# Performance work log

Hardware: AMD Instinct MI355X
Metric: run time of the kernel (lower is better)

The kernel has to match this reference:

```python
import jax, jax.numpy as jnp
import numpy as np

ALPHA = 0.2        # LeakyReLU negative slope
MASK_VAL = -9e15   # matches torch -9000000000000000.0


def setup_inputs() -> dict:
    key = jax.random.key(0)
    k_h, k_adj, k_w, k_a = jax.random.split(key, 4)
    B, N, Nodes, IF, OF = 8, 8, 512, 256, 256
    h = jax.random.normal(k_h, (B, N, Nodes, IF), dtype=jnp.float32)
    adj = jax.random.randint(k_adj, (Nodes, Nodes), 0, 2, dtype=jnp.int32)
    # xavier_uniform with gain=1.414
    gain = 1.414
    lim_w = gain * np.sqrt(6.0 / (IF + OF))
    W = jax.random.uniform(k_w, (IF, OF), dtype=jnp.float32, minval=-lim_w, maxval=lim_w)
    lim_a = gain * np.sqrt(6.0 / (2 * OF + 1))
    a = jax.random.uniform(k_a, (2 * OF, 1), dtype=jnp.float32, minval=-lim_a, maxval=lim_a)
    return {"h": h, "adj": adj, "W": W, "a": a}


def reference(h, adj, W, a):
    # Wh: [B, N, Nodes, OF]
    Wh = jnp.matmul(h, W)
    OF = W.shape[1]
    a1, a2 = a[:OF, 0], a[OF:, 0]
    # e[..., i, j] = leakyrelu(a1 . Wh_i + a2 . Wh_j)  (decomposed additive attention)
    src = jnp.einsum('bnif,f->bni', Wh, a1)  # [B, N, Nodes]
    dst = jnp.einsum('bnjf,f->bnj', Wh, a2)  # [B, N, Nodes]
    e = jax.nn.leaky_relu(src[..., :, None] + dst[..., None, :], negative_slope=ALPHA)
    attention = jnp.where(adj > 0, e, jnp.full_like(e, MASK_VAL))
    attention = jax.nn.softmax(attention, axis=-1)
    # dropout is identity in eval mode (training=False)
    h_prime = jnp.matmul(attention, Wh)  # [B, N, Nodes, OF]
    return jax.nn.elu(h_prime)  # concat=True
```

## Files before the change

### kernel.cpp

```cpp
#include <hip/hip_runtime.h>
#include <hip/hip_bf16.h>


#define ALPHA 0.2f
#define MASK_VAL -9000000000000000.0f
#define NODES 512
#define FDIM 256
#define BN 64

typedef float  f32x4 __attribute__((ext_vector_type(4)));
typedef int    i32x4 __attribute__((ext_vector_type(4)));
typedef short  s16x8 __attribute__((ext_vector_type(8)));
typedef short  s16x4 __attribute__((ext_vector_type(4)));
typedef __bf16 bf16x8 __attribute__((ext_vector_type(8)));

__device__ __forceinline__ unsigned short f2bfu(float x) {
    __hip_bfloat16 b = __float2bfloat16(x);
    unsigned short u; __builtin_memcpy(&u, &b, 2); return u;
}
__device__ __forceinline__ float bfu2f(unsigned short u) {
    unsigned int w = ((unsigned int)u) << 16; return __uint_as_float(w);
}
__device__ __forceinline__ f32x4 mfma16(s16x8 a, s16x8 b, f32x4 c) {
    return __builtin_amdgcn_mfma_f32_16x16x32_bf16(
        __builtin_bit_cast(bf16x8, a), __builtin_bit_cast(bf16x8, b), c, 0, 0, 0);
}

__device__ __forceinline__ void split8v(f32x4 v0, f32x4 v1, s16x8& hi, s16x8& lo)
{
    float x[8] = {v0[0], v0[1], v0[2], v0[3], v1[0], v1[1], v1[2], v1[3]};
    unsigned hw[4], lw[4];
    #pragma unroll
    for (int d = 0; d < 4; ++d) {
        const unsigned u0 = __float_as_uint(x[2*d]);
        const unsigned u1 = __float_as_uint(x[2*d + 1]);
        hw[d] = __builtin_amdgcn_perm(u1, u0, 0x07060302);
        const float l0 = x[2*d]     - __uint_as_float(u0 & 0xFFFF0000u);
        const float l1 = x[2*d + 1] - __uint_as_float(u1 & 0xFFFF0000u);
        lw[d] = __builtin_amdgcn_perm(__float_as_uint(l1), __float_as_uint(l0),
                                      0x07060302);
    }
    hi = __builtin_bit_cast(s16x8, *(unsigned(*)[4])hw);
    lo = __builtin_bit_cast(s16x8, *(unsigned(*)[4])lw);
}

__device__ __forceinline__ void gll16(const void* g, void* l) {
    __builtin_amdgcn_global_load_lds(
        (const __attribute__((address_space(1))) unsigned int*)g,
        (__attribute__((address_space(3))) unsigned int*)l,
        16, 0, 0);
}

__global__ __launch_bounds__(256) void detect_kernel(const unsigned short* __restrict__ hraw,
                                                     int* __restrict__ flag)
{
    const int tid = threadIdx.x;
    float m = 0.0f;
    for (int i = tid; i < 16384; i += 256) {
        unsigned int w = ((unsigned int)hraw[i]) << 16;
        float v = __uint_as_float(w);
        v = fabsf(v);
        if (!(v == v)) v = 1e30f;
        m = fmaxf(m, v);
    }
    #pragma unroll
    for (int off = 32; off >= 1; off >>= 1)
        m = fmaxf(m, __shfl_down(m, off));
    __shared__ float red[4];
    if ((tid & 63) == 0) red[tid >> 6] = m;
    __syncthreads();
    if (tid == 0) {
        float mm = fmaxf(fmaxf(red[0], red[1]), fmaxf(red[2], red[3]));
        *flag = (mm > 1e4f) ? 1 : 0;
    }
}

__global__ __launch_bounds__(256) void prep_w_kernel(
    const void* __restrict__ Wv, const int* __restrict__ flagp,
    short* __restrict__ WtHi, short* __restrict__ WtLo)
{
    const int flag = *flagp;
    __shared__ float tile[16][17];
    const int tx = threadIdx.x & 15, ty = threadIdx.x >> 4;
    const int kk = blockIdx.y * 16 + ty;
    const int f  = blockIdx.x * 16 + tx;
    float v;
    if (flag) v = ((const float*)Wv)[kk * FDIM + f];
    else      v = bfu2f(((const unsigned short*)Wv)[kk * FDIM + f]);
    tile[ty][tx] = v;
    __syncthreads();
    const float x = tile[tx][ty];
    const int fo = blockIdx.x * 16 + ty;
    const int ko = blockIdx.y * 16 + tx;
    unsigned short h = f2bfu(x);
    WtHi[fo * FDIM + ko] = (short)h;
    WtLo[fo * FDIM + ko] = (short)f2bfu(x - bfu2f(h));
}

__global__ __launch_bounds__(512, 4) void wh_gemm(
    const void* __restrict__ hv,
    const short* __restrict__ WtHi, const short* __restrict__ WtLo,
    const void* __restrict__ av, const int* __restrict__ flagp,
    short* __restrict__ WhTHi, short* __restrict__ WhTLo,
    float* __restrict__ srcv, float* __restrict__ dstv)
{
    __shared__ __align__(16) char smem[69632];

    const int flag = *flagp;
    const int blk = blockIdx.x;
    const int bn  = blk >> 3;
    const int i0  = (blk & 7) * 64;
    const size_t r0g = (size_t)blk * 64;
    const int tid = threadIdx.x;
    const int w = tid >> 6, l = tid & 63;
    const int fb = l & 15, g = l >> 4;

    if (flag) {
        const int srow = tid >> 3, q = tid & 7;
        const float* gA = (const float*)hv + (r0g + srow) * FDIM;
        #pragma unroll
        for (int i = 0; i < 4; ++i) {
            const int seg = q + 8 * i;
            f32x4 v0 = *(const f32x4*)(gA + seg * 8);
            f32x4 v1 = *(const f32x4*)(gA + seg * 8 + 4);
            s16x8 hi, lo; split8v(v0, v1, hi, lo);
            const int slot = seg ^ (srow & 7);
            *(s16x8*)(smem + srow * 512 + slot * 16) = hi;
            *(s16x8*)(smem + 32768 + srow * 512 + slot * 16) = lo;
        }
    } else {
        const short* hs = (const short*)hv;
        const unsigned wub = (unsigned)(tid & ~63);
        #pragma unroll
        for (int i = 0; i < 4; ++i) {
            const int idx = i * 512 + tid;
            const int row = idx >> 5, slot = idx & 31;
            const int srcseg = slot ^ (row & 7);
            gll16(hs + (r0g + row) * FDIM + srcseg * 8,
                  smem + (i * 512 + (int)wub) * 16);
        }
    }
    __syncthreads();

    f32x4 acc[4][2];
    #pragma unroll
    for (int rt = 0; rt < 4; ++rt)
        #pragma unroll
        for (int ct = 0; ct < 2; ++ct) acc[rt][ct] = f32x4{0.f,0.f,0.f,0.f};

    const int f0 = w * 32 + fb;
    const int f1 = f0 + 16;
    const short* gH0 = WtHi + f0 * FDIM + g * 8;
    const short* gH1 = WtHi + f1 * FDIM + g * 8;
    const short* gL0 = WtLo + f0 * FDIM + g * 8;
    const short* gL1 = WtLo + f1 * FDIM + g * 8;

    if (flag) {
        s16x8 pb[3][4];
        #pragma unroll
        for (int d = 0; d < 2; ++d) {
            pb[d][0] = *(const s16x8*)(gH0 + d * 32);
            pb[d][1] = *(const s16x8*)(gH1 + d * 32);
            pb[d][2] = *(const s16x8*)(gL0 + d * 32);
            pb[d][3] = *(const s16x8*)(gL1 + d * 32);
        }
        #pragma unroll
        for (int t = 0; t < 8; ++t) {
            const int cur = t % 3;
            if (t + 2 < 8) {
                const int nx = (t + 2) % 3;
                pb[nx][0] = *(const s16x8*)(gH0 + (t + 2) * 32);
                pb[nx][1] = *(const s16x8*)(gH1 + (t + 2) * 32);
                pb[nx][2] = *(const s16x8*)(gL0 + (t + 2) * 32);
                pb[nx][3] = *(const s16x8*)(gL1 + (t + 2) * 32);
            }
            s16x8 ah[4], al[4];
            #pragma unroll
            for (int rt = 0; rt < 4; ++rt) {
                const int row = rt * 16 + fb;
                const int slot = (t * 4 + g) ^ (row & 7);
                ah[rt] = *(const s16x8*)(smem + row * 512 + slot * 16);
                al[rt] = *(const s16x8*)(smem + 32768 + row * 512 + slot * 16);
            }
            __builtin_amdgcn_s_setprio(1);
            #pragma unroll
            for (int rt = 0; rt < 4; ++rt) {
                acc[rt][0] = mfma16(ah[rt], pb[cur][0], acc[rt][0]);
                acc[rt][0] = mfma16(al[rt], pb[cur][0], acc[rt][0]);
                acc[rt][0] = mfma16(ah[rt], pb[cur][2], acc[rt][0]);
                acc[rt][1] = mfma16(ah[rt], pb[cur][1], acc[rt][1]);
                acc[rt][1] = mfma16(al[rt], pb[cur][1], acc[rt][1]);
                acc[rt][1] = mfma16(ah[rt], pb[cur][3], acc[rt][1]);
            }
            __builtin_amdgcn_s_setprio(0);
        }
    } else {
        s16x8 pb[3][2];
        #pragma unroll
        for (int d = 0; d < 2; ++d) {
            pb[d][0] = *(const s16x8*)(gH0 + d * 32);
            pb[d][1] = *(const s16x8*)(gH1 + d * 32);
        }
        #pragma unroll
        for (int t = 0; t < 8; ++t) {
            const int cur = t % 3;
            if (t + 2 < 8) {
                const int nx = (t + 2) % 3;
                pb[nx][0] = *(const s16x8*)(gH0 + (t + 2) * 32);
                pb[nx][1] = *(const s16x8*)(gH1 + (t + 2) * 32);
            }
            s16x8 ah[4];
            #pragma unroll
            for (int rt = 0; rt < 4; ++rt) {
                const int row = rt * 16 + fb;
                const int slot = (t * 4 + g) ^ (row & 7);
                ah[rt] = *(const s16x8*)(smem + row * 512 + slot * 16);
            }
            __builtin_amdgcn_s_setprio(1);
            #pragma unroll
            for (int rt = 0; rt < 4; ++rt) {
                acc[rt][0] = mfma16(ah[rt], pb[cur][0], acc[rt][0]);
                acc[rt][1] = mfma16(ah[rt], pb[cur][1], acc[rt][1]);
            }
            __builtin_amdgcn_s_setprio(0);
        }
    }

    const size_t wbT = (size_t)bn * FDIM * NODES;
    #pragma unroll
    for (int rt = 0; rt < 4; ++rt) {
        const int orow = i0 + rt * 16 + g * 4;
        #pragma unroll
        for (int ct = 0; ct < 2; ++ct) {
            const int f = w * 32 + ct * 16 + fb;
            s16x4 h4, l4;
            #pragma unroll
            for (int r = 0; r < 4; ++r) {
                float x = acc[rt][ct][r];
                unsigned short hh = f2bfu(x);
                h4[r] = (short)hh;
                l4[r] = (short)f2bfu(x - bfu2f(hh));
            }
            *(s16x4*)(WhTHi + wbT + (size_t)f * NODES + orow) = h4;
            *(s16x4*)(WhTLo + wbT + (size_t)f * NODES + orow) = l4;
        }
    }

    float a1v[2], a2v[2];
    #pragma unroll
    for (int ct = 0; ct < 2; ++ct) {
        const int f = w * 32 + ct * 16 + fb;
        if (flag) {
            a1v[ct] = ((const float*)av)[f];
            a2v[ct] = ((const float*)av)[FDIM + f];
        } else {
            a1v[ct] = bfu2f(((const unsigned short*)av)[f]);
            a2v[ct] = bfu2f(((const unsigned short*)av)[FDIM + f]);
        }
    }
    float* red1 = (float*)(smem + 65536);
    float* red2 = (float*)(smem + 67584);
    #pragma unroll
    for (int rt = 0; rt < 4; ++rt) {
        #pragma unroll
        for (int r = 0; r < 4; ++r) {
            float s1 = 0.f, s2 = 0.f;
            #pragma unroll
            for (int ct = 0; ct < 2; ++ct) {
                s1 = fmaf(acc[rt][ct][r], a1v[ct], s1);
                s2 = fmaf(acc[rt][ct][r], a2v[ct], s2);
            }
            #pragma unroll
            for (int off = 1; off <= 8; off <<= 1) {
                s1 += __shfl_xor(s1, off);
                s2 += __shfl_xor(s2, off);
            }
            if (fb == 0) {
                red1[w * 64 + rt * 16 + g * 4 + r] = s1;
                red2[w * 64 + rt * 16 + g * 4 + r] = s2;
            }
        }
    }
    __syncthreads();
    if (tid < 64) {
        float s1 = 0.f, s2 = 0.f;
        #pragma unroll
        for (int ww = 0; ww < 8; ++ww) {
            s1 += red1[ww * 64 + tid];
            s2 += red2[ww * 64 + tid];
        }
        srcv[bn * NODES + i0 + tid] = s1;
        dstv[bn * NODES + i0 + tid] = s2;
    }
}

__global__ __launch_bounds__(512, 4) void pv_gemm(
    const short* __restrict__ WhTHi, const short* __restrict__ WhTLo,
    const float* __restrict__ srcv, const float* __restrict__ dstv,
    const int* __restrict__ adj, const int* __restrict__ flagp,
    void* __restrict__ out)
{
    __shared__ __align__(16) char smem[65536];

    const int flag = *flagp;
    const int b0 = blockIdx.x;
    const int blk = (b0 & 7) * 64 + (b0 >> 3);
    const int bn  = blk >> 3;
    const int i0  = (blk & 7) * 64;
    const int tid = threadIdx.x;
    const int w = tid >> 6, l = tid & 63;

    const short* bhig = WhTHi + (size_t)bn * FDIM * NODES;
    const short* blog = WhTLo + (size_t)bn * FDIM * NODES;

    {
        const float* drow = dstv + bn * NODES;
        const int j = l * 8;
        for (int rr = 0; rr < 8; ++rr) {
            const int r = w * 8 + rr;
            const int* adjrow = adj + (size_t)(i0 + r) * NODES;
            const float srow = srcv[bn * NODES + i0 + r];
            const i32x4 q0 = *(const i32x4*)(adjrow + j);
            const i32x4 q1 = *(const i32x4*)(adjrow + j + 4);
            const f32x4 d0 = *(const f32x4*)(drow + j);
            const f32x4 d1 = *(const f32x4*)(drow + j + 4);
            float e[8];
            #pragma unroll
            for (int k = 0; k < 4; ++k) {
                float ev = srow + d0[k];
                ev = (ev > 0.f) ? ev : ALPHA * ev;
                e[k] = (q0[k] > 0) ? ev : MASK_VAL;
                float ew = srow + d1[k];
                ew = (ew > 0.f) ? ew : ALPHA * ew;
                e[4 + k] = (q1[k] > 0) ? ew : MASK_VAL;
            }
            float m = e[0];
            #pragma unroll
            for (int k = 1; k < 8; ++k) m = fmaxf(m, e[k]);
            #pragma unroll
            for (int off = 1; off <= 32; off <<= 1) m = fmaxf(m, __shfl_xor(m, off));
            float p[8], s = 0.f;
            #pragma unroll
            for (int k = 0; k < 8; ++k) {
                p[k] = __expf(e[k] - m);
                s += p[k];
            }
            #pragma unroll
            for (int off = 1; off <= 32; off <<= 1) s += __shfl_xor(s, off);
            const float isum = 1.0f / s;
            s16x8 ph;
            #pragma unroll
            for (int k = 0; k < 8; ++k) ph[k] = (short)f2bfu(p[k] * isum);
            *(s16x8*)(smem + r * 1024 + ((l ^ (r & 7)) * 16)) = ph;
        }
    }
    __syncthreads();

    const int fb = l & 15, g = l >> 4;
    const int f0 = w * 32 + fb;
    const int f1 = f0 + 16;
    const short* gH0 = bhig + (size_t)f0 * NODES + g * 8;
    const short* gH1 = bhig + (size_t)f1 * NODES + g * 8;
    const short* gL0 = blog + (size_t)f0 * NODES + g * 8;
    const short* gL1 = blog + (size_t)f1 * NODES + g * 8;

    f32x4 acc[4][2];
    #pragma unroll
    for (int rt = 0; rt < 4; ++rt)
        #pragma unroll
        for (int ct = 0; ct < 2; ++ct) acc[rt][ct] = f32x4{0.f,0.f,0.f,0.f};

    s16x8 pb[3][4];
    #pragma unroll
    for (int d = 0; d < 2; ++d) {
        pb[d][0] = *(const s16x8*)(gH0 + d * 32);
        pb[d][1] = *(const s16x8*)(gH1 + d * 32);
        pb[d][2] = *(const s16x8*)(gL0 + d * 32);
        pb[d][3] = *(const s16x8*)(gL1 + d * 32);
    }
    #pragma unroll
    for (int t = 0; t < 16; ++t) {
        const int cur = t % 3;
        if (t + 2 < 16) {
            const int nx = (t + 2) % 3;
            pb[nx][0] = *(const s16x8*)(gH0 + (t + 2) * 32);
            pb[nx][1] = *(const s16x8*)(gH1 + (t + 2) * 32);
            pb[nx][2] = *(const s16x8*)(gL0 + (t + 2) * 32);
            pb[nx][3] = *(const s16x8*)(gL1 + (t + 2) * 32);
        }
        s16x8 af[4];
        #pragma unroll
        for (int rt = 0; rt < 4; ++rt) {
            const int row = rt * 16 + fb;
            const unsigned seg = (unsigned)(t * 4 + g) ^ (unsigned)(row & 7);
            af[rt] = *(const s16x8*)(smem + (unsigned)(row * 1024) + seg * 16);
        }
        __builtin_amdgcn_s_setprio(1);
        #pragma unroll
        for (int rt = 0; rt < 4; ++rt) {
            acc[rt][0] = mfma16(af[rt], pb[cur][0], acc[rt][0]);
            acc[rt][0] = mfma16(af[rt], pb[cur][2], acc[rt][0]);
            acc[rt][1] = mfma16(af[rt], pb[cur][1], acc[rt][1]);
            acc[rt][1] = mfma16(af[rt], pb[cur][3], acc[rt][1]);
        }
        __builtin_amdgcn_s_setprio(0);
    }

    #pragma unroll
    for (int rt = 0; rt < 4; ++rt) {
        #pragma unroll
        for (int ct = 0; ct < 2; ++ct) {
            const int f = w * 32 + ct * 16 + fb;
            #pragma unroll
            for (int r = 0; r < 4; ++r) {
                float v = acc[rt][ct][r];
                v = (v > 0.f) ? v : expm1f(v);
                const size_t o = ((size_t)bn * NODES + i0 + rt * 16 + g * 4 + r) * FDIM + f;
                if (flag) ((float*)out)[o] = v;
                else      ((unsigned short*)out)[o] = f2bfu(v);
            }
        }
    }
}

extern "C" void kernel_launch(void* const* d_in, const int* in_sizes, int n_in,
                              void* d_out, int out_size, void* d_ws, size_t ws_size,
                              hipStream_t stream)
{
    const void* h   = d_in[0];
    const int*  adj = (const int*)d_in[1];
    const void* W   = d_in[2];
    const void* a   = d_in[3];

    int*   flag  = (int*)d_ws;
    float* srcv  = (float*)d_ws + 64;
    float* dstv  = srcv + BN * NODES;
    short* WtHi  = (short*)(dstv + BN * NODES);
    short* WtLo  = WtHi + FDIM * FDIM;
    short* WhTHi = WtLo + FDIM * FDIM;
    short* WhTLo = WhTHi + (size_t)BN * FDIM * NODES;

    detect_kernel<<<1, 256, 0, stream>>>((const unsigned short*)h, flag);
    prep_w_kernel<<<dim3(16, 16), 256, 0, stream>>>(W, flag, WtHi, WtLo);
    wh_gemm<<<512, 512, 0, stream>>>(h, WtHi, WtLo, a, flag,
                                     WhTHi, WhTLo, srcv, dstv);
    pv_gemm<<<512, 512, 0, stream>>>(WhTHi, WhTLo, srcv, dstv, adj, flag, d_out);
}
```

Measured before the change: 167.4 us.

## Defer softmax normalization to epilogue and restructure per-row softmax mapping

The softmax prologue in pv_gemm now gives each row to 8 threads, each covering 64 columns, in place of one wavefront per row looping over 8 rows. Unnormalized exponentials are written to LDS as bf16, and the reciprocal row sum is stored in a small LDS array and applied to the accumulator in the epilogue. The first Wh tile prefetch is also issued before the softmax, so global loads overlap with it. Together these drop the wide 64-lane shuffle reductions and a per-element multiply. The cost is reading adj and dst twice (once for the max, once for the exponentials) and bf16 rounding of unnormalized probabilities, whose values stay within (0,1].

Measured after the change: 178.2 us. +6.5%, slower.

```diff
diff --git a/kernel.cpp b/kernel.cpp
--- a/kernel.cpp
+++ b/kernel.cpp
@@ -300,7 +300,7 @@
     const int* __restrict__ adj, const int* __restrict__ flagp,
     void* __restrict__ out)
 {
-    __shared__ __align__(16) char smem[65536];
+    __shared__ __align__(16) char smem[65792];
 
     const int flag = *flagp;
     const int b0 = blockIdx.x;
@@ -309,52 +309,10 @@
     const int i0  = (blk & 7) * 64;
     const int tid = threadIdx.x;
     const int w = tid >> 6, l = tid & 63;
+    float* rowinvS = (float*)(smem + 65536);
 
     const short* bhig = WhTHi + (size_t)bn * FDIM * NODES;
     const short* blog = WhTLo + (size_t)bn * FDIM * NODES;
-
-    {
-        const float* drow = dstv + bn * NODES;
-        const int j = l * 8;
-        for (int rr = 0; rr < 8; ++rr) {
-            const int r = w * 8 + rr;
-            const int* adjrow = adj + (size_t)(i0 + r) * NODES;
-            const float srow = srcv[bn * NODES + i0 + r];
-            const i32x4 q0 = *(const i32x4*)(adjrow + j);
-            const i32x4 q1 = *(const i32x4*)(adjrow + j + 4);
-            const f32x4 d0 = *(const f32x4*)(drow + j);
-            const f32x4 d1 = *(const f32x4*)(drow + j + 4);
-            float e[8];
-            #pragma unroll
-            for (int k = 0; k < 4; ++k) {
-                float ev = srow + d0[k];
-                ev = (ev > 0.f) ? ev : ALPHA * ev;
-                e[k] = (q0[k] > 0) ? ev : MASK_VAL;
-                float ew = srow + d1[k];
-                ew = (ew > 0.f) ? ew : ALPHA * ew;
-                e[4 + k] = (q1[k] > 0) ? ew : MASK_VAL;
-            }
-            float m = e[0];
-            #pragma unroll
-            for (int k = 1; k < 8; ++k) m = fmaxf(m, e[k]);
-            #pragma unroll
-            for (int off = 1; off <= 32; off <<= 1) m = fmaxf(m, __shfl_xor(m, off));
-            float p[8], s = 0.f;
-            #pragma unroll
-            for (int k = 0; k < 8; ++k) {
-                p[k] = __expf(e[k] - m);
-                s += p[k];
-            }
-            #pragma unroll
-            for (int off = 1; off <= 32; off <<= 1) s += __shfl_xor(s, off);
-            const float isum = 1.0f / s;
-            s16x8 ph;
-            #pragma unroll
-            for (int k = 0; k < 8; ++k) ph[k] = (short)f2bfu(p[k] * isum);
-            *(s16x8*)(smem + r * 1024 + ((l ^ (r & 7)) * 16)) = ph;
-        }
-    }
-    __syncthreads();
 
     const int fb = l & 15, g = l >> 4;
     const int f0 = w * 32 + fb;
@@ -364,12 +322,6 @@
     const short* gL0 = blog + (size_t)f0 * NODES + g * 8;
     const short* gL1 = blog + (size_t)f1 * NODES + g * 8;
 
-    f32x4 acc[4][2];
-    #pragma unroll
-    for (int rt = 0; rt < 4; ++rt)
-        #pragma unroll
-        for (int ct = 0; ct < 2; ++ct) acc[rt][ct] = f32x4{0.f,0.f,0.f,0.f};
-
     s16x8 pb[3][4];
     #pragma unroll
     for (int d = 0; d < 2; ++d) {
@@ -378,6 +330,68 @@
         pb[d][2] = *(const s16x8*)(gL0 + d * 32);
         pb[d][3] = *(const s16x8*)(gL1 + d * 32);
     }
+
+    {
+        const int row = tid >> 3, sub = tid & 7;
+        const int* adjrow = adj + (size_t)(i0 + row) * NODES + sub * 64;
+        const float* drow = dstv + bn * NODES + sub * 64;
+        const float srow = srcv[bn * NODES + i0 + row];
+
+        float m = -3.0e38f;
+        #pragma unroll
+        for (int c = 0; c < 16; ++c) {
+            const i32x4 q = *(const i32x4*)(adjrow + c * 4);
+            const f32x4 d = *(const f32x4*)(drow + c * 4);
+            #pragma unroll
+            for (int e = 0; e < 4; ++e) {
+                float ev = srow + d[e];
+                ev = (ev > 0.f) ? ev : ALPHA * ev;
+                m = fmaxf(m, (q[e] > 0) ? ev : MASK_VAL);
+            }
+        }
+        m = fmaxf(m, __shfl_xor(m, 1));
+        m = fmaxf(m, __shfl_xor(m, 2));
+        m = fmaxf(m, __shfl_xor(m, 4));
+
+        float s = 0.f;
+        #pragma unroll
+        for (int c8 = 0; c8 < 8; ++c8) {
+            const i32x4 q0 = *(const i32x4*)(adjrow + c8 * 8);
+            const i32x4 q1 = *(const i32x4*)(adjrow + c8 * 8 + 4);
+            const f32x4 d0 = *(const f32x4*)(drow + c8 * 8);
+            const f32x4 d1 = *(const f32x4*)(drow + c8 * 8 + 4);
+            s16x8 ph;
+            #pragma unroll
+            for (int e = 0; e < 4; ++e) {
+                float ev = srow + d0[e];
+                ev = (ev > 0.f) ? ev : ALPHA * ev;
+                ev = (q0[e] > 0) ? ev : MASK_VAL;
+                float p = __expf(ev - m);
+                s += p;
+                ph[e] = (short)f2bfu(p);
+                float ew = srow + d1[e];
+                ew = (ew > 0.f) ? ew : ALPHA * ew;
+                ew = (q1[e] > 0) ? ew : MASK_VAL;
+                float p2 = __expf(ew - m);
+                s += p2;
+                ph[4 + e] = (short)f2bfu(p2);
+            }
+            const int slot = (sub * 8 + c8) ^ (row & 7);
+            *(s16x8*)(smem + row * 1024 + slot * 16) = ph;
+        }
+        s += __shfl_xor(s, 1);
+        s += __shfl_xor(s, 2);
+        s += __shfl_xor(s, 4);
+        if (sub == 0) rowinvS[row] = 1.0f / s;
+    }
+    __syncthreads();
+
+    f32x4 acc[4][2];
+    #pragma unroll
+    for (int rt = 0; rt < 4; ++rt)
+        #pragma unroll
+        for (int ct = 0; ct < 2; ++ct) acc[rt][ct] = f32x4{0.f,0.f,0.f,0.f};
+
     #pragma unroll
     for (int t = 0; t < 16; ++t) {
         const int cur = t % 3;
@@ -408,12 +422,15 @@
 
     #pragma unroll
     for (int rt = 0; rt < 4; ++rt) {
+        float inv[4];
+        #pragma unroll
+        for (int r = 0; r < 4; ++r) inv[r] = rowinvS[rt * 16 + g * 4 + r];
         #pragma unroll
         for (int ct = 0; ct < 2; ++ct) {
             const int f = w * 32 + ct * 16 + fb;
             #pragma unroll
             for (int r = 0; r < 4; ++r) {
-                float v = acc[rt][ct][r];
+                float v = acc[rt][ct][r] * inv[r];
                 v = (v > 0.f) ? v : expm1f(v);
                 const size_t o = ((size_t)bn * NODES + i0 + rt * 16 + g * 4 + r) * FDIM + f;
                 if (flag) ((float*)out)[o] = v;
```
